# Optimization experiments

Hardware: AMD Instinct MI355X
Metric: run time of the kernel (lower is better)

Reference implementation:

```python
import jax, jax.numpy as jnp
import numpy as np

B, C, N = 2, 32, 4096
EPS = 1e-5


def _batchnorm1d(x, gamma, bias):
    # BatchNorm1d in training mode: stats over (batch, spatial) per channel, biased var
    mean = x.mean(axis=(0, 2), keepdims=True)
    var = x.var(axis=(0, 2), keepdims=True)
    return (x - mean) * jax.lax.rsqrt(var + EPS) * gamma[None, :, None] + bias[None, :, None]


def setup_inputs() -> dict:
    key = jax.random.key(0)
    k1, k2, k3 = jax.random.split(key, 3)
    Feature = jax.random.normal(k1, (B, C, N), dtype=jnp.float32)
    gamma = jnp.ones((C,), dtype=jnp.float32)
    bn_bias = jnp.zeros((C,), dtype=jnp.float32)
    alpha = jax.random.uniform(k2, (), dtype=jnp.float32)
    beta = jax.random.uniform(k3, (), dtype=jnp.float32)
    return {"Feature": Feature, "gamma": gamma, "bn_bias": bn_bias, "alpha": alpha, "beta": beta}


def reference(Feature, gamma, bn_bias, alpha, beta):
    a = Feature                                   # [B, C, N]
    # --- PAM: BN + ReLU prologue, then spatial N x N attention ---
    f = jax.nn.relu(_batchnorm1d(Feature, gamma, bn_bias))
    cb = jnp.einsum('bcn,bcm->bnm', f, f)         # c^T c : [B, N, N]
    s = jax.nn.softmax(cb, axis=1)                # softmax over dim=1 (as in source)
    e_p = jnp.einsum('bcn,bmn->bcm', f, s)        # c @ s^T : [B, C, N]
    pam = alpha * e_p + a
    # --- CAM: channel C x C attention, softmax over batch axis (dim=0 as in source) ---
    aa = jnp.einsum('bcn,bdn->bdc', a, a)         # matmul(a, a^T).permute(0,2,1) : [B, C, C]
    x = jax.nn.softmax(aa, axis=0)
    e_c = jnp.einsum('bji,bjn->bin', x, a)        # x^T @ a : [B, C, N]
    cam = beta * e_c + a
    return pam + cam
```

## Files before the change

### kernel.cpp

```cpp
#include <hip/hip_runtime.h>
#include <math.h>


#define BB 2
#define CC 32
#define NN 4096
#define EPSV 1e-5f

typedef short short8 __attribute__((ext_vector_type(8)));
typedef float f32x4 __attribute__((ext_vector_type(4)));

#define OFF_FNC  0
#define OFF_FCN  131072
#define OFF_M    262144
#define OFF_SC   270336
#define OFF_SH   270368
#define OFF_AA   270400
#define OFF_XW   272448
#define OFF_Z    274496
#define OFF_EP   282688
#define WS_FLOATS 544832

__device__ inline ushort f2bf(float x) {
    uint u = __float_as_uint(x);
    uint r = u + 0x7FFFu + ((u >> 16) & 1u);
    return (ushort)(r >> 16);
}
__device__ inline float bf2f(ushort h) { return __uint_as_float(((uint)h) << 16); }
__device__ inline uint packbf(float lo, float hi) {
    return (__float_as_uint(hi) & 0xFFFF0000u) | (__float_as_uint(lo) >> 16);
}

__global__ void k_pre(const float* __restrict__ x, const float* __restrict__ gamma,
                      const float* __restrict__ bias, float* __restrict__ ws) {
    __shared__ float rs[4], rs2[4];
    __shared__ float red[4][CC];
    const int tid = threadIdx.x;
    const int w = tid >> 6, l = tid & 63;
    if (blockIdx.x < 32) {
        const int c = blockIdx.x;
        float s = 0.f, s2 = 0.f;
        for (int i = tid; i < BB * NN; i += 256) {
            const int b = i >> 12, n = i & (NN - 1);
            const float v = x[((size_t)(b * CC + c)) * NN + n];
            s += v; s2 += v * v;
        }
        for (int off = 32; off; off >>= 1) { s += __shfl_down(s, off); s2 += __shfl_down(s2, off); }
        if (l == 0) { rs[w] = s; rs2[w] = s2; }
        __syncthreads();
        if (tid == 0) {
            const float S = rs[0] + rs[1] + rs[2] + rs[3];
            const float S2 = rs2[0] + rs2[1] + rs2[2] + rs2[3];
            const float mean = S * (1.f / (BB * NN));
            const float var = S2 * (1.f / (BB * NN)) - mean * mean;
            const float sc = gamma[c] * rsqrtf(var + EPSV);
            ws[OFF_SC + c] = sc;
            ws[OFF_SH + c] = bias[c] - mean * sc;
        }
    } else {
        const int bid = blockIdx.x - 32;
        const int b = bid >> 5, d = bid & 31;
        const float* xb = x + (size_t)b * CC * NN;
        float acc[CC];
        #pragma unroll
        for (int c = 0; c < CC; ++c) acc[c] = 0.f;
        for (int n = tid; n < NN; n += 256) {
            const float vd = xb[(size_t)d * NN + n];
            #pragma unroll
            for (int c = 0; c < CC; ++c) acc[c] += xb[(size_t)c * NN + n] * vd;
        }
        #pragma unroll
        for (int c = 0; c < CC; ++c) {
            float r = acc[c];
            for (int off = 32; off; off >>= 1) r += __shfl_down(r, off);
            if (l == 0) red[w][c] = r;
        }
        __syncthreads();
        if (tid < CC) ws[OFF_AA + ((size_t)(b * CC + d)) * CC + tid] =
            red[0][tid] + red[1][tid] + red[2][tid] + red[3][tid];
    }
}

__global__ void k_makef(const float* __restrict__ x, float* __restrict__ ws) {
    const int idx = blockIdx.x * 256 + threadIdx.x;
    const int b = idx >> 12, n = idx & (NN - 1);
    __shared__ float ssc[CC], ssh[CC];
    if (threadIdx.x < CC) { ssc[threadIdx.x] = ws[OFF_SC + threadIdx.x]; ssh[threadIdx.x] = ws[OFF_SH + threadIdx.x]; }
    __syncthreads();
    ushort* fnc = (ushort*)(ws + OFF_FNC) + (size_t)idx * CC;
    ushort* fcn = (ushort*)(ws + OFF_FCN);
    float msum = 0.f;
    #pragma unroll
    for (int c = 0; c < CC; ++c) {
        const float v = x[((size_t)(b * CC + c)) * NN + n];
        const float f = fmaxf(v * ssc[c] + ssh[c], 0.f);
        const ushort h = f2bf(f);
        const float fr = bf2f(h);
        msum += fr * fr;
        fnc[c] = h;
        fcn[((size_t)(b * CC + c)) * NN + n] = h;
    }
    ws[OFF_M + idx] = msum;
}

__global__ void __launch_bounds__(256) k_zpass(float* __restrict__ ws) {
    if (blockIdx.x == 512) {
        for (int t = threadIdx.x; t < CC * CC; t += 256) {
            const int i = t >> 5, j = t & 31;
            const float a0 = ws[OFF_AA + (0 * CC + j) * CC + i];
            const float a1 = ws[OFF_AA + (1 * CC + j) * CC + i];
            const float mx = fmaxf(a0, a1);
            const float e0 = __expf(a0 - mx), e1 = __expf(a1 - mx);
            const float inv = 1.f / (e0 + e1);
            ws[OFF_XW + (0 * CC + i) * CC + j] = e0 * inv;
            ws[OFF_XW + (1 * CC + i) * CC + j] = e1 * inv;
        }
        return;
    }
    const ushort* fnc = (const ushort*)(ws + OFF_FNC);
    const int bid = blockIdx.x;
    const int b   = bid >> 8;
    const int ng  = (bid >> 3) & 31;
    const int mch = bid & 7;
    const int lane = threadIdx.x & 63;
    const int wv   = threadIdx.x >> 6;
    const int ml = lane & 15, kg = lane >> 4;
    const int nbA = ng * 128 + wv * 16;
    const int nbB = nbA + 64;
    const f32x4 zero = {0.f, 0.f, 0.f, 0.f};
    const short8 bfA = *(const short8*)(fnc + ((size_t)(b * NN + nbA + ml)) * CC + kg * 8);
    const short8 bfB = *(const short8*)(fnc + ((size_t)(b * NN + nbB + ml)) * CC + kg * 8);
    const float MA = ws[OFF_M + b * NN + nbA + ml];
    const float MB = ws[OFF_M + b * NN + nbB + ml];
    float zA = 0.f, zB = 0.f;
    const int m0 = mch * 512;
    for (int mm = m0; mm < m0 + 512; mm += 16) {
        const short8 af = *(const short8*)(fnc + ((size_t)(b * NN + mm + ml)) * CC + kg * 8);
        f32x4 dA = __builtin_amdgcn_mfma_f32_16x16x32_bf16(af, bfA, zero, 0, 0, 0);
        f32x4 dB = __builtin_amdgcn_mfma_f32_16x16x32_bf16(af, bfB, zero, 0, 0, 0);
        zA += __expf(dA[0] - MA) + __expf(dA[1] - MA) + __expf(dA[2] - MA) + __expf(dA[3] - MA);
        zB += __expf(dB[0] - MB) + __expf(dB[1] - MB) + __expf(dB[2] - MB) + __expf(dB[3] - MB);
    }
    zA += __shfl_xor(zA, 16); zA += __shfl_xor(zA, 32);
    zB += __shfl_xor(zB, 16); zB += __shfl_xor(zB, 32);
    if (lane < 16) {
        atomicAdd(ws + OFF_Z + b * NN + nbA + ml, zA);
        atomicAdd(ws + OFF_Z + b * NN + nbB + ml, zB);
    }
}

__global__ void k_zinv(float* __restrict__ ws) {
    const int i = blockIdx.x * 256 + threadIdx.x;
    ws[OFF_Z + i] = 1.f / ws[OFF_Z + i];
}

__global__ void __launch_bounds__(256) k_eppass(float* __restrict__ ws) {
    const ushort* fnc = (const ushort*)(ws + OFF_FNC);
    const ushort* fcn = (const ushort*)(ws + OFF_FCN);
    const int bid = blockIdx.x;
    const int b   = bid >> 8;
    const int mg  = (bid >> 2) & 63;
    const int nch = bid & 3;
    const int lane = threadIdx.x & 63;
    const int wv   = threadIdx.x >> 6;
    const int ml = lane & 15, kg = lane >> 4;
    const int mb = mg * 64 + wv * 16;
    const f32x4 zero = {0.f, 0.f, 0.f, 0.f};
    const short8 bm = *(const short8*)(fnc + ((size_t)(b * NN + mb + ml)) * CC + kg * 8);
    f32x4 acc0 = zero, acc1 = zero;
    const float* Mp  = ws + OFF_M + b * NN;
    const float* Zip = ws + OFF_Z + b * NN;
    const int n0beg = nch * 1024;
    for (int n0 = n0beg; n0 < n0beg + 1024; n0 += 32) {
        const short8 an0 = *(const short8*)(fnc + ((size_t)(b * NN + n0      + ml)) * CC + kg * 8);
        const short8 an1 = *(const short8*)(fnc + ((size_t)(b * NN + n0 + 16 + ml)) * CC + kg * 8);
        f32x4 d0 = __builtin_amdgcn_mfma_f32_16x16x32_bf16(an0, bm, zero, 0, 0, 0);
        f32x4 d1 = __builtin_amdgcn_mfma_f32_16x16x32_bf16(an1, bm, zero, 0, 0, 0);
        const float4 M0 = *(const float4*)(Mp  + n0 + kg * 4);
        const float4 M1 = *(const float4*)(Mp  + n0 + 16 + kg * 4);
        const float4 Z0 = *(const float4*)(Zip + n0 + kg * 4);
        const float4 Z1 = *(const float4*)(Zip + n0 + 16 + kg * 4);
        const float w00 = __expf(d0[0] - M0.x) * Z0.x;
        const float w01 = __expf(d0[1] - M0.y) * Z0.y;
        const float w02 = __expf(d0[2] - M0.z) * Z0.z;
        const float w03 = __expf(d0[3] - M0.w) * Z0.w;
        const float w10 = __expf(d1[0] - M1.x) * Z1.x;
        const float w11 = __expf(d1[1] - M1.y) * Z1.y;
        const float w12 = __expf(d1[2] - M1.z) * Z1.z;
        const float w13 = __expf(d1[3] - M1.w) * Z1.w;
        const uint p0 = packbf(w00, w01), p1 = packbf(w02, w03);
        const uint q0 = packbf(w10, w11), q1 = packbf(w12, w13);
        union { uint u[4]; short8 s; } wf;
        {
            const int s0 = (((kg & 1) << 1) + 0) * 16 + ml;
            const int s1 = (((kg & 1) << 1) + 1) * 16 + ml;
            const uint vp0 = __shfl(p0, s0), vp1 = __shfl(p1, s0);
            const uint vp2 = __shfl(p0, s1), vp3 = __shfl(p1, s1);
            const uint vq0 = __shfl(q0, s0), vq1 = __shfl(q1, s0);
            const uint vq2 = __shfl(q0, s1), vq3 = __shfl(q1, s1);
            const bool hi = (kg >= 2);
            wf.u[0] = hi ? vq0 : vp0; wf.u[1] = hi ? vq1 : vp1;
            wf.u[2] = hi ? vq2 : vp2; wf.u[3] = hi ? vq3 : vp3;
        }
        const short8 a20 = *(const short8*)(fcn + ((size_t)(b * CC + ml))      * NN + n0 + kg * 8);
        const short8 a21 = *(const short8*)(fcn + ((size_t)(b * CC + 16 + ml)) * NN + n0 + kg * 8);
        acc0 = __builtin_amdgcn_mfma_f32_16x16x32_bf16(a20, wf.s, acc0, 0, 0, 0);
        acc1 = __builtin_amdgcn_mfma_f32_16x16x32_bf16(a21, wf.s, acc1, 0, 0, 0);
    }
    #pragma unroll
    for (int r = 0; r < 4; ++r) {
        atomicAdd(ws + OFF_EP + ((size_t)(b * CC + kg * 4 + r))      * NN + mb + ml, acc0[r]);
        atomicAdd(ws + OFF_EP + ((size_t)(b * CC + 16 + kg * 4 + r)) * NN + mb + ml, acc1[r]);
    }
}

__global__ void k_final(const float* __restrict__ x, const float* __restrict__ alpha_p,
                        const float* __restrict__ beta_p, const float* __restrict__ ws,
                        float* __restrict__ out) {
    const int idx = blockIdx.x * 128 + threadIdx.x;
    const int b = idx >> 12, m = idx & (NN - 1);
    __shared__ float sxw[CC * CC];
    for (int i = threadIdx.x; i < CC * CC; i += 128)
        sxw[i] = ws[OFF_XW + b * CC * CC + i];
    __syncthreads();
    const float alpha = *alpha_p, beta = *beta_p;
    float ec[CC];
    #pragma unroll
    for (int c = 0; c < CC; ++c) ec[c] = 0.f;
    const float* xb = x + (size_t)b * CC * NN;
    #pragma unroll
    for (int j = 0; j < CC; ++j) {
        const float aj = xb[(size_t)j * NN + m];
        #pragma unroll
        for (int c = 0; c < CC; ++c) ec[c] += sxw[c * CC + j] * aj;
    }
    #pragma unroll
    for (int c = 0; c < CC; ++c) {
        const float av = xb[(size_t)c * NN + m];
        out[((size_t)(b * CC + c)) * NN + m] =
            alpha * ws[OFF_EP + ((size_t)(b * CC + c)) * NN + m] + beta * ec[c] + 2.f * av;
    }
}

extern "C" void kernel_launch(void* const* d_in, const int* in_sizes, int n_in,
                              void* d_out, int out_size, void* d_ws, size_t ws_size,
                              hipStream_t stream) {
    const float* x     = (const float*)d_in[0];
    const float* gamma = (const float*)d_in[1];
    const float* bias  = (const float*)d_in[2];
    const float* alpha = (const float*)d_in[3];
    const float* beta  = (const float*)d_in[4];
    float* out = (float*)d_out;
    float* ws  = (float*)d_ws;

    hipMemsetAsync((char*)d_ws + (size_t)OFF_Z * 4, 0, (size_t)(8192 + 262144) * 4, stream);

    hipLaunchKernelGGL(k_pre,    dim3(96),  dim3(256), 0, stream, x, gamma, bias, ws);
    hipLaunchKernelGGL(k_makef,  dim3(32),  dim3(256), 0, stream, x, ws);
    hipLaunchKernelGGL(k_zpass,  dim3(513), dim3(256), 0, stream, ws);
    hipLaunchKernelGGL(k_zinv,   dim3(32),  dim3(256), 0, stream, ws);
    hipLaunchKernelGGL(k_eppass, dim3(512), dim3(256), 0, stream, ws);
    hipLaunchKernelGGL(k_final,  dim3(64),  dim3(128), 0, stream, x, alpha, beta, ws, out);
}
```

Baseline: 140.9 us.

## Fuse all stages into one persistent kernel with grid-wide barriers

Replaces the six separate launches with one 512-block kernel that separates the stages with atomic-counter grid barriers. The channel Gram matrix moves to shared-memory tiles with partial sums, the makef and final stages are spread across all 512 blocks instead of 32 or 64, and zeroing of the accumulators moves into the kernel. The z-inverse kernel is dropped in favour of rcp at the use site. This removes launch gaps and raises parallelism in the small stages, but it depends on all 512 blocks being resident at once or the barrier deadlocks.

```diff
diff --git a/kernel.cpp b/kernel.cpp
--- a/kernel.cpp
+++ b/kernel.cpp
@@ -6,6 +6,7 @@
 #define CC 32
 #define NN 4096
 #define EPSV 1e-5f
+#define NBLK 512
 
 typedef short short8 __attribute__((ext_vector_type(8)));
 typedef float f32x4 __attribute__((ext_vector_type(4)));
@@ -15,11 +16,13 @@
 #define OFF_M    262144
 #define OFF_SC   270336
 #define OFF_SH   270368
-#define OFF_AA   270400
-#define OFF_XW   272448
-#define OFF_Z    274496
-#define OFF_EP   282688
-#define WS_FLOATS 544832
+#define OFF_XW   270400
+#define OFF_AAP  272448
+#define OFF_Z    305216
+#define OFF_EP   313408
+#define OFF_CNT  575552
+#define ZERO_BASE 305216
+#define ZERO_N4   67584
 
 __device__ inline ushort f2bf(float x) {
     uint u = __float_as_uint(x);
@@ -31,214 +34,223 @@
     return (__float_as_uint(hi) & 0xFFFF0000u) | (__float_as_uint(lo) >> 16);
 }
 
-__global__ void k_pre(const float* __restrict__ x, const float* __restrict__ gamma,
-                      const float* __restrict__ bias, float* __restrict__ ws) {
-    __shared__ float rs[4], rs2[4];
-    __shared__ float red[4][CC];
-    const int tid = threadIdx.x;
-    const int w = tid >> 6, l = tid & 63;
-    if (blockIdx.x < 32) {
-        const int c = blockIdx.x;
+__device__ inline void gsync(uint* cnt, uint target) {
+    __threadfence();
+    __syncthreads();
+    if (threadIdx.x == 0) {
+        atomicAdd(cnt, 1u);
+        while (atomicAdd(cnt, 0u) < target) __builtin_amdgcn_s_sleep(1);
+    }
+    __syncthreads();
+    __threadfence();
+}
+
+__global__ void __launch_bounds__(256, 2)
+k_dam(const float* __restrict__ x, const float* __restrict__ gamma,
+      const float* __restrict__ bias, const float* __restrict__ alpha_p,
+      const float* __restrict__ beta_p, float* __restrict__ ws,
+      float* __restrict__ out) {
+    __shared__ float smem[4352];
+    const int blk = blockIdx.x, t = threadIdx.x;
+    const int lane = t & 63, wv = t >> 6;
+    const int ml = lane & 15, kg = lane >> 4;
+    const f32x4 fzero = {0.f, 0.f, 0.f, 0.f};
+    uint* cnt = (uint*)(ws + OFF_CNT);
+
+    if (blk < 32) {
+        const int c = blk;
         float s = 0.f, s2 = 0.f;
-        for (int i = tid; i < BB * NN; i += 256) {
-            const int b = i >> 12, n = i & (NN - 1);
-            const float v = x[((size_t)(b * CC + c)) * NN + n];
+        for (int i = t; i < BB * NN; i += 256) {
+            const int bb = i >> 12, n = i & (NN - 1);
+            const float v = x[((size_t)(bb * CC + c)) * NN + n];
             s += v; s2 += v * v;
         }
         for (int off = 32; off; off >>= 1) { s += __shfl_down(s, off); s2 += __shfl_down(s2, off); }
-        if (l == 0) { rs[w] = s; rs2[w] = s2; }
+        if (lane == 0) { smem[wv] = s; smem[4 + wv] = s2; }
         __syncthreads();
-        if (tid == 0) {
-            const float S = rs[0] + rs[1] + rs[2] + rs[3];
-            const float S2 = rs2[0] + rs2[1] + rs2[2] + rs2[3];
+        if (t == 0) {
+            const float S = smem[0] + smem[1] + smem[2] + smem[3];
+            const float S2 = smem[4] + smem[5] + smem[6] + smem[7];
             const float mean = S * (1.f / (BB * NN));
             const float var = S2 * (1.f / (BB * NN)) - mean * mean;
             const float sc = gamma[c] * rsqrtf(var + EPSV);
             ws[OFF_SC + c] = sc;
             ws[OFF_SH + c] = bias[c] - mean * sc;
         }
+    } else if (blk < 64) {
+        const int blk2 = blk - 32;
+        const int b = blk2 >> 4, chnk = blk2 & 15;
+        const int nb = chnk * 256;
+        const int d = t >> 3, cg4 = (t & 7) * 4;
+        float a0 = 0.f, a1 = 0.f, a2 = 0.f, a3 = 0.f;
+        for (int it = 0; it < 2; ++it) {
+            __syncthreads();
+            for (int li = t; li < 4096; li += 256) {
+                const int row = li >> 7, col = li & 127;
+                smem[row * 132 + col] = x[((size_t)(b * CC + row)) * NN + nb + it * 128 + col];
+            }
+            __syncthreads();
+            for (int k = 0; k < 128; ++k) {
+                const float vd = smem[d * 132 + k];
+                a0 += smem[(cg4 + 0) * 132 + k] * vd;
+                a1 += smem[(cg4 + 1) * 132 + k] * vd;
+                a2 += smem[(cg4 + 2) * 132 + k] * vd;
+                a3 += smem[(cg4 + 3) * 132 + k] * vd;
+            }
+        }
+        float* dst = ws + OFF_AAP + ((size_t)((b * 16 + chnk) * CC + d)) * CC + cg4;
+        dst[0] = a0; dst[1] = a1; dst[2] = a2; dst[3] = a3;
     } else {
-        const int bid = blockIdx.x - 32;
-        const int b = bid >> 5, d = bid & 31;
-        const float* xb = x + (size_t)b * CC * NN;
-        float acc[CC];
+        for (int gid = (blk - 64) * 256 + t; gid < ZERO_N4; gid += 448 * 256)
+            ((float4*)(ws + ZERO_BASE))[gid] = make_float4(0.f, 0.f, 0.f, 0.f);
+    }
+    gsync(cnt, 1 * NBLK);
+
+    {
+        const int ch = t & 31;
+        const float sc = ws[OFF_SC + ch], sh = ws[OFF_SH + ch];
         #pragma unroll
-        for (int c = 0; c < CC; ++c) acc[c] = 0.f;
-        for (int n = tid; n < NN; n += 256) {
-            const float vd = xb[(size_t)d * NN + n];
+        for (int it = 0; it < 2; ++it) {
+            const int col = (t >> 5) + it * 8;
+            const int idx = blk * 16 + col;
+            const int b = idx >> 12, n = idx & (NN - 1);
+            const float v = x[((size_t)(b * CC + ch)) * NN + n];
+            const float f = fmaxf(v * sc + sh, 0.f);
+            const ushort h = f2bf(f);
+            const float fr = bf2f(h);
+            ((ushort*)(ws + OFF_FNC))[(size_t)idx * CC + ch] = h;
+            ((ushort*)(ws + OFF_FCN))[((size_t)(b * CC + ch)) * NN + n] = h;
+            float s = fr * fr;
+            s += __shfl_xor(s, 1); s += __shfl_xor(s, 2); s += __shfl_xor(s, 4);
+            s += __shfl_xor(s, 8); s += __shfl_xor(s, 16);
+            if (ch == 0) ws[OFF_M + idx] = s;
+        }
+        if (blk == 511) {
+            for (int li = t; li < CC * CC; li += 256) {
+                const int i = li >> 5, j = li & 31;
+                float q0 = 0.f, q1 = 0.f;
+                for (int cchunk = 0; cchunk < 16; ++cchunk) {
+                    q0 += ws[OFF_AAP + ((size_t)((0 * 16 + cchunk) * CC + j)) * CC + i];
+                    q1 += ws[OFF_AAP + ((size_t)((1 * 16 + cchunk) * CC + j)) * CC + i];
+                }
+                const float mx = fmaxf(q0, q1);
+                const float e0 = __expf(q0 - mx), e1 = __expf(q1 - mx);
+                const float inv = 1.f / (e0 + e1);
+                ws[OFF_XW + 0 * 1024 + i * 32 + j] = e0 * inv;
+                ws[OFF_XW + 1 * 1024 + i * 32 + j] = e1 * inv;
+            }
+        }
+    }
+    gsync(cnt, 2 * NBLK);
+
+    {
+        const ushort* fnc = (const ushort*)(ws + OFF_FNC);
+        const int b = blk >> 8;
+        const int rem = blk & 255;
+        const int ng = rem >> 3, mch = rem & 7;
+        const int nbA = ng * 128 + wv * 16, nbB = nbA + 64;
+        const short8 bfA = *(const short8*)(fnc + ((size_t)(b * NN + nbA + ml)) * CC + kg * 8);
+        const short8 bfB = *(const short8*)(fnc + ((size_t)(b * NN + nbB + ml)) * CC + kg * 8);
+        const float MA = ws[OFF_M + b * NN + nbA + ml];
+        const float MB = ws[OFF_M + b * NN + nbB + ml];
+        float zA = 0.f, zB = 0.f;
+        const int m0 = mch * 512;
+        for (int mm = m0; mm < m0 + 512; mm += 16) {
+            const short8 af = *(const short8*)(fnc + ((size_t)(b * NN + mm + ml)) * CC + kg * 8);
+            f32x4 dA = __builtin_amdgcn_mfma_f32_16x16x32_bf16(af, bfA, fzero, 0, 0, 0);
+            f32x4 dB = __builtin_amdgcn_mfma_f32_16x16x32_bf16(af, bfB, fzero, 0, 0, 0);
+            zA += __expf(dA[0] - MA) + __expf(dA[1] - MA) + __expf(dA[2] - MA) + __expf(dA[3] - MA);
+            zB += __expf(dB[0] - MB) + __expf(dB[1] - MB) + __expf(dB[2] - MB) + __expf(dB[3] - MB);
+        }
+        zA += __shfl_xor(zA, 16); zA += __shfl_xor(zA, 32);
+        zB += __shfl_xor(zB, 16); zB += __shfl_xor(zB, 32);
+        if (lane < 16) {
+            atomicAdd(ws + OFF_Z + b * NN + nbA + ml, zA);
+            atomicAdd(ws + OFF_Z + b * NN + nbB + ml, zB);
+        }
+    }
+    gsync(cnt, 3 * NBLK);
+
+    {
+        const ushort* fnc = (const ushort*)(ws + OFF_FNC);
+        const ushort* fcn = (const ushort*)(ws + OFF_FCN);
+        const int b = blk >> 8;
+        const int rem = blk & 255;
+        const int mg = rem >> 2, nch = rem & 3;
+        const int mb = mg * 64 + wv * 16;
+        const short8 bm = *(const short8*)(fnc + ((size_t)(b * NN + mb + ml)) * CC + kg * 8);
+        f32x4 acc0 = fzero, acc1 = fzero;
+        const float* Mp = ws + OFF_M + b * NN;
+        const float* Zp = ws + OFF_Z + b * NN;
+        const int n0beg = nch * 1024;
+        for (int n0 = n0beg; n0 < n0beg + 1024; n0 += 32) {
+            const short8 an0 = *(const short8*)(fnc + ((size_t)(b * NN + n0      + ml)) * CC + kg * 8);
+            const short8 an1 = *(const short8*)(fnc + ((size_t)(b * NN + n0 + 16 + ml)) * CC + kg * 8);
+            f32x4 d0 = __builtin_amdgcn_mfma_f32_16x16x32_bf16(an0, bm, fzero, 0, 0, 0);
+            f32x4 d1 = __builtin_amdgcn_mfma_f32_16x16x32_bf16(an1, bm, fzero, 0, 0, 0);
+            const float4 M0 = *(const float4*)(Mp + n0 + kg * 4);
+            const float4 M1 = *(const float4*)(Mp + n0 + 16 + kg * 4);
+            const float4 Z0 = *(const float4*)(Zp + n0 + kg * 4);
+            const float4 Z1 = *(const float4*)(Zp + n0 + 16 + kg * 4);
+            const float w00 = __expf(d0[0] - M0.x) * __builtin_amdgcn_rcpf(Z0.x);
+            const float w01 = __expf(d0[1] - M0.y) * __builtin_amdgcn_rcpf(Z0.y);
+            const float w02 = __expf(d0[2] - M0.z) * __builtin_amdgcn_rcpf(Z0.z);
+            const float w03 = __expf(d0[3] - M0.w) * __builtin_amdgcn_rcpf(Z0.w);
+            const float w10 = __expf(d1[0] - M1.x) * __builtin_amdgcn_rcpf(Z1.x);
+            const float w11 = __expf(d1[1] - M1.y) * __builtin_amdgcn_rcpf(Z1.y);
+            const float w12 = __expf(d1[2] - M1.z) * __builtin_amdgcn_rcpf(Z1.z);
+            const float w13 = __expf(d1[3] - M1.w) * __builtin_amdgcn_rcpf(Z1.w);
+            const uint p0 = packbf(w00, w01), p1 = packbf(w02, w03);
+            const uint q0 = packbf(w10, w11), q1 = packbf(w12, w13);
+            union { uint u[4]; short8 s; } wf;
+            {
+                const int s0 = (((kg & 1) << 1) + 0) * 16 + ml;
+                const int s1 = (((kg & 1) << 1) + 1) * 16 + ml;
+                const uint vp0 = __shfl(p0, s0), vp1 = __shfl(p1, s0);
+                const uint vp2 = __shfl(p0, s1), vp3 = __shfl(p1, s1);
+                const uint vq0 = __shfl(q0, s0), vq1 = __shfl(q1, s0);
+                const uint vq2 = __shfl(q0, s1), vq3 = __shfl(q1, s1);
+                const bool hi = (kg >= 2);
+                wf.u[0] = hi ? vq0 : vp0; wf.u[1] = hi ? vq1 : vp1;
+                wf.u[2] = hi ? vq2 : vp2; wf.u[3] = hi ? vq3 : vp3;
+            }
+            const short8 a20 = *(const short8*)(fcn + ((size_t)(b * CC + ml))      * NN + n0 + kg * 8);
+            const short8 a21 = *(const short8*)(fcn + ((size_t)(b * CC + 16 + ml)) * NN + n0 + kg * 8);
+            acc0 = __builtin_amdgcn_mfma_f32_16x16x32_bf16(a20, wf.s, acc0, 0, 0, 0);
+            acc1 = __builtin_amdgcn_mfma_f32_16x16x32_bf16(a21, wf.s, acc1, 0, 0, 0);
+        }
+        #pragma unroll
+        for (int r = 0; r < 4; ++r) {
+            atomicAdd(ws + OFF_EP + ((size_t)(b * CC + kg * 4 + r))      * NN + mb + ml, acc0[r]);
+            atomicAdd(ws + OFF_EP + ((size_t)(b * CC + 16 + kg * 4 + r)) * NN + mb + ml, acc1[r]);
+        }
+    }
+    gsync(cnt, 4 * NBLK);
+
+    {
+        const float alpha = *alpha_p, beta = *beta_p;
+        float* sa = smem;
+        float* sxw = smem + 256;
+        const int base = blk * 16;
+        const int b = base >> 12;
+        for (int li = t; li < CC * CC; li += 256)
+            sxw[(li >> 5) * 33 + (li & 31)] = ws[OFF_XW + b * 1024 + li];
+        const int k = t >> 5, c = t & 31;
+        #pragma unroll
+        for (int it = 0; it < 2; ++it) {
+            const int m0 = (base + it * 8) & (NN - 1);
+            __syncthreads();
+            { const int j = t >> 3, kc = t & 7;
+              sa[j * 8 + kc] = x[((size_t)(b * CC + j)) * NN + m0 + kc]; }
+            __syncthreads();
+            const int m = m0 + k;
+            float ec = 0.f;
             #pragma unroll
-            for (int c = 0; c < CC; ++c) acc[c] += xb[(size_t)c * NN + n] * vd;
-        }
-        #pragma unroll
-        for (int c = 0; c < CC; ++c) {
-            float r = acc[c];
-            for (int off = 32; off; off >>= 1) r += __shfl_down(r, off);
-            if (l == 0) red[w][c] = r;
-        }
-        __syncthreads();
-        if (tid < CC) ws[OFF_AA + ((size_t)(b * CC + d)) * CC + tid] =
-            red[0][tid] + red[1][tid] + red[2][tid] + red[3][tid];
-    }
-}
-
-__global__ void k_makef(const float* __restrict__ x, float* __restrict__ ws) {
-    const int idx = blockIdx.x * 256 + threadIdx.x;
-    const int b = idx >> 12, n = idx & (NN - 1);
-    __shared__ float ssc[CC], ssh[CC];
-    if (threadIdx.x < CC) { ssc[threadIdx.x] = ws[OFF_SC + threadIdx.x]; ssh[threadIdx.x] = ws[OFF_SH + threadIdx.x]; }
-    __syncthreads();
-    ushort* fnc = (ushort*)(ws + OFF_FNC) + (size_t)idx * CC;
-    ushort* fcn = (ushort*)(ws + OFF_FCN);
-    float msum = 0.f;
-    #pragma unroll
-    for (int c = 0; c < CC; ++c) {
-        const float v = x[((size_t)(b * CC + c)) * NN + n];
-        const float f = fmaxf(v * ssc[c] + ssh[c], 0.f);
-        const ushort h = f2bf(f);
-        const float fr = bf2f(h);
-        msum += fr * fr;
-        fnc[c] = h;
-        fcn[((size_t)(b * CC + c)) * NN + n] = h;
-    }
-    ws[OFF_M + idx] = msum;
-}
-
-__global__ void __launch_bounds__(256) k_zpass(float* __restrict__ ws) {
-    if (blockIdx.x == 512) {
-        for (int t = threadIdx.x; t < CC * CC; t += 256) {
-            const int i = t >> 5, j = t & 31;
-            const float a0 = ws[OFF_AA + (0 * CC + j) * CC + i];
-            const float a1 = ws[OFF_AA + (1 * CC + j) * CC + i];
-            const float mx = fmaxf(a0, a1);
-            const float e0 = __expf(a0 - mx), e1 = __expf(a1 - mx);
-            const float inv = 1.f / (e0 + e1);
-            ws[OFF_XW + (0 * CC + i) * CC + j] = e0 * inv;
-            ws[OFF_XW + (1 * CC + i) * CC + j] = e1 * inv;
-        }
-        return;
-    }
-    const ushort* fnc = (const ushort*)(ws + OFF_FNC);
-    const int bid = blockIdx.x;
-    const int b   = bid >> 8;
-    const int ng  = (bid >> 3) & 31;
-    const int mch = bid & 7;
-    const int lane = threadIdx.x & 63;
-    const int wv   = threadIdx.x >> 6;
-    const int ml = lane & 15, kg = lane >> 4;
-    const int nbA = ng * 128 + wv * 16;
-    const int nbB = nbA + 64;
-    const f32x4 zero = {0.f, 0.f, 0.f, 0.f};
-    const short8 bfA = *(const short8*)(fnc + ((size_t)(b * NN + nbA + ml)) * CC + kg * 8);
-    const short8 bfB = *(const short8*)(fnc + ((size_t)(b * NN + nbB + ml)) * CC + kg * 8);
-    const float MA = ws[OFF_M + b * NN + nbA + ml];
-    const float MB = ws[OFF_M + b * NN + nbB + ml];
-    float zA = 0.f, zB = 0.f;
-    const int m0 = mch * 512;
-    for (int mm = m0; mm < m0 + 512; mm += 16) {
-        const short8 af = *(const short8*)(fnc + ((size_t)(b * NN + mm + ml)) * CC + kg * 8);
-        f32x4 dA = __builtin_amdgcn_mfma_f32_16x16x32_bf16(af, bfA, zero, 0, 0, 0);
-        f32x4 dB = __builtin_amdgcn_mfma_f32_16x16x32_bf16(af, bfB, zero, 0, 0, 0);
-        zA += __expf(dA[0] - MA) + __expf(dA[1] - MA) + __expf(dA[2] - MA) + __expf(dA[3] - MA);
-        zB += __expf(dB[0] - MB) + __expf(dB[1] - MB) + __expf(dB[2] - MB) + __expf(dB[3] - MB);
-    }
-    zA += __shfl_xor(zA, 16); zA += __shfl_xor(zA, 32);
-    zB += __shfl_xor(zB, 16); zB += __shfl_xor(zB, 32);
-    if (lane < 16) {
-        atomicAdd(ws + OFF_Z + b * NN + nbA + ml, zA);
-        atomicAdd(ws + OFF_Z + b * NN + nbB + ml, zB);
-    }
-}
-
-__global__ void k_zinv(float* __restrict__ ws) {
-    const int i = blockIdx.x * 256 + threadIdx.x;
-    ws[OFF_Z + i] = 1.f / ws[OFF_Z + i];
-}
-
-__global__ void __launch_bounds__(256) k_eppass(float* __restrict__ ws) {
-    const ushort* fnc = (const ushort*)(ws + OFF_FNC);
-    const ushort* fcn = (const ushort*)(ws + OFF_FCN);
-    const int bid = blockIdx.x;
-    const int b   = bid >> 8;
-    const int mg  = (bid >> 2) & 63;
-    const int nch = bid & 3;
-    const int lane = threadIdx.x & 63;
-    const int wv   = threadIdx.x >> 6;
-    const int ml = lane & 15, kg = lane >> 4;
-    const int mb = mg * 64 + wv * 16;
-    const f32x4 zero = {0.f, 0.f, 0.f, 0.f};
-    const short8 bm = *(const short8*)(fnc + ((size_t)(b * NN + mb + ml)) * CC + kg * 8);
-    f32x4 acc0 = zero, acc1 = zero;
-    const float* Mp  = ws + OFF_M + b * NN;
-    const float* Zip = ws + OFF_Z + b * NN;
-    const int n0beg = nch * 1024;
-    for (int n0 = n0beg; n0 < n0beg + 1024; n0 += 32) {
-        const short8 an0 = *(const short8*)(fnc + ((size_t)(b * NN + n0      + ml)) * CC + kg * 8);
-        const short8 an1 = *(const short8*)(fnc + ((size_t)(b * NN + n0 + 16 + ml)) * CC + kg * 8);
-        f32x4 d0 = __builtin_amdgcn_mfma_f32_16x16x32_bf16(an0, bm, zero, 0, 0, 0);
-        f32x4 d1 = __builtin_amdgcn_mfma_f32_16x16x32_bf16(an1, bm, zero, 0, 0, 0);
-        const float4 M0 = *(const float4*)(Mp  + n0 + kg * 4);
-        const float4 M1 = *(const float4*)(Mp  + n0 + 16 + kg * 4);
-        const float4 Z0 = *(const float4*)(Zip + n0 + kg * 4);
-        const float4 Z1 = *(const float4*)(Zip + n0 + 16 + kg * 4);
-        const float w00 = __expf(d0[0] - M0.x) * Z0.x;
-        const float w01 = __expf(d0[1] - M0.y) * Z0.y;
-        const float w02 = __expf(d0[2] - M0.z) * Z0.z;
-        const float w03 = __expf(d0[3] - M0.w) * Z0.w;
-        const float w10 = __expf(d1[0] - M1.x) * Z1.x;
-        const float w11 = __expf(d1[1] - M1.y) * Z1.y;
-        const float w12 = __expf(d1[2] - M1.z) * Z1.z;
-        const float w13 = __expf(d1[3] - M1.w) * Z1.w;
-        const uint p0 = packbf(w00, w01), p1 = packbf(w02, w03);
-        const uint q0 = packbf(w10, w11), q1 = packbf(w12, w13);
-        union { uint u[4]; short8 s; } wf;
-        {
-            const int s0 = (((kg & 1) << 1) + 0) * 16 + ml;
-            const int s1 = (((kg & 1) << 1) + 1) * 16 + ml;
-            const uint vp0 = __shfl(p0, s0), vp1 = __shfl(p1, s0);
-            const uint vp2 = __shfl(p0, s1), vp3 = __shfl(p1, s1);
-            const uint vq0 = __shfl(q0, s0), vq1 = __shfl(q1, s0);
-            const uint vq2 = __shfl(q0, s1), vq3 = __shfl(q1, s1);
-            const bool hi = (kg >= 2);
-            wf.u[0] = hi ? vq0 : vp0; wf.u[1] = hi ? vq1 : vp1;
-            wf.u[2] = hi ? vq2 : vp2; wf.u[3] = hi ? vq3 : vp3;
-        }
-        const short8 a20 = *(const short8*)(fcn + ((size_t)(b * CC + ml))      * NN + n0 + kg * 8);
-        const short8 a21 = *(const short8*)(fcn + ((size_t)(b * CC + 16 + ml)) * NN + n0 + kg * 8);
-        acc0 = __builtin_amdgcn_mfma_f32_16x16x32_bf16(a20, wf.s, acc0, 0, 0, 0);
-        acc1 = __builtin_amdgcn_mfma_f32_16x16x32_bf16(a21, wf.s, acc1, 0, 0, 0);
-    }
-    #pragma unroll
-    for (int r = 0; r < 4; ++r) {
-        atomicAdd(ws + OFF_EP + ((size_t)(b * CC + kg * 4 + r))      * NN + mb + ml, acc0[r]);
-        atomicAdd(ws + OFF_EP + ((size_t)(b * CC + 16 + kg * 4 + r)) * NN + mb + ml, acc1[r]);
-    }
-}
-
-__global__ void k_final(const float* __restrict__ x, const float* __restrict__ alpha_p,
-                        const float* __restrict__ beta_p, const float* __restrict__ ws,
-                        float* __restrict__ out) {
-    const int idx = blockIdx.x * 128 + threadIdx.x;
-    const int b = idx >> 12, m = idx & (NN - 1);
-    __shared__ float sxw[CC * CC];
-    for (int i = threadIdx.x; i < CC * CC; i += 128)
-        sxw[i] = ws[OFF_XW + b * CC * CC + i];
-    __syncthreads();
-    const float alpha = *alpha_p, beta = *beta_p;
-    float ec[CC];
-    #pragma unroll
-    for (int c = 0; c < CC; ++c) ec[c] = 0.f;
-    const float* xb = x + (size_t)b * CC * NN;
-    #pragma unroll
-    for (int j = 0; j < CC; ++j) {
-        const float aj = xb[(size_t)j * NN + m];
-        #pragma unroll
-        for (int c = 0; c < CC; ++c) ec[c] += sxw[c * CC + j] * aj;
-    }
-    #pragma unroll
-    for (int c = 0; c < CC; ++c) {
-        const float av = xb[(size_t)c * NN + m];
-        out[((size_t)(b * CC + c)) * NN + m] =
-            alpha * ws[OFF_EP + ((size_t)(b * CC + c)) * NN + m] + beta * ec[c] + 2.f * av;
+            for (int j = 0; j < CC; ++j) ec += sxw[c * 33 + j] * sa[j * 8 + k];
+            const float av = sa[c * 8 + k];
+            const float ep = ws[OFF_EP + ((size_t)(b * CC + c)) * NN + m];
+            out[((size_t)(b * CC + c)) * NN + m] = alpha * ep + beta * ec + 2.f * av;
+        }
     }
 }
 
@@ -253,12 +265,8 @@
     float* out = (float*)d_out;
     float* ws  = (float*)d_ws;
 
-    hipMemsetAsync((char*)d_ws + (size_t)OFF_Z * 4, 0, (size_t)(8192 + 262144) * 4, stream);
-
-    hipLaunchKernelGGL(k_pre,    dim3(96),  dim3(256), 0, stream, x, gamma, bias, ws);
-    hipLaunchKernelGGL(k_makef,  dim3(32),  dim3(256), 0, stream, x, ws);
-    hipLaunchKernelGGL(k_zpass,  dim3(513), dim3(256), 0, stream, ws);
-    hipLaunchKernelGGL(k_zinv,   dim3(32),  dim3(256), 0, stream, ws);
-    hipLaunchKernelGGL(k_eppass, dim3(512), dim3(256), 0, stream, ws);
-    hipLaunchKernelGGL(k_final,  dim3(64),  dim3(128), 0, stream, x, alpha, beta, ws, out);
-}
+    hipMemsetAsync((char*)d_ws + (size_t)OFF_CNT * 4, 0, 256, stream);
+
+    hipLaunchKernelGGL(k_dam, dim3(NBLK), dim3(256), 0, stream,
+                       x, gamma, bias, alpha, beta, ws, out);
+}
```

Result: slower. 496.7 us (+252.5%).
